# Performance work log

Hardware: AMD Instinct MI355X
Metric: run time of the kernel (lower is better)

The kernel has to match this reference:

```python
import jax, jax.numpy as jnp
import numpy as np

R_ITER = 3
EPS = 1e-7  # keras.backend.epsilon()


def squash(v, axis=-1):
    s2 = jnp.sum(jnp.square(v), axis=axis, keepdims=True)
    scale = s2 / (1.0 + s2) / jnp.sqrt(s2 + EPS)
    return scale * v


def setup_inputs() -> dict:
    key = jax.random.key(0)
    kx, kw = jax.random.split(key)
    B, N_IN, D_IN = 64, 2048, 8
    N_OUT, D_OUT = 32, 16
    x = jax.random.normal(kx, (B, N_IN, D_IN), dtype=jnp.float32)
    # W matches keras weight (1, N_IN//shared, N_OUT, D_OUT, D_IN) with shared=1,
    # stored here without the leading broadcast dim. RandomNormal(stddev=0.1).
    W = 0.1 * jax.random.normal(kw, (N_IN, N_OUT, D_OUT, D_IN), dtype=jnp.float32)
    return {"x": x, "W": W}


def reference(x, W):
    # predictions u_hat[b, i, j, :] = W[i, j] @ x[b, i]  -> [B, N_in, N_out, D_out]
    preds = jnp.einsum('nodi,bni->bnod', W, x)
    N_in, N_out = preds.shape[1], preds.shape[2]
    # raw routing logits start at zeros with broadcast batch dim (as in TF code)
    raw = jnp.zeros((1, N_in, N_out), dtype=x.dtype)
    for i in range(R_ITER):
        rw = jax.nn.softmax(raw, axis=2)                      # softmax over output caps
        s = jnp.sum(rw[..., None] * preds, axis=1)            # [B, N_out, D_out]
        v = squash(s, axis=-1)                                # squash over capsule dim
        if i < R_ITER - 1:
            # agreement: <u_hat_ij, v_j>
            raw = raw + jnp.einsum('bnod,bod->bno', preds, v)
    return v, rw
```

## Files before the change

kernel.cpp:

```cpp
#include <hip/hip_runtime.h>

static constexpr int B_    = 64;
static constexpr int N_    = 2048;
static constexpr int DI_   = 8;
static constexpr int O_    = 32;
static constexpr int P_    = 16;
static constexpr int OP_   = O_ * P_;
static constexpr int M_    = OP_ * B_;
static constexpr int CHUNK_ = 8;
static constexpr int NBLK_  = N_ / CHUNK_;

template <int MODE, bool ATOMIC>
__global__ __launch_bounds__(1024, 4)
void fused_pass(const float* __restrict__ x, const float* __restrict__ W,
                const float* __restrict__ v_in, float* __restrict__ s_out,
                float* __restrict__ rw_out) {
  __shared__ float x_lds[CHUNK_ * 8 * 65];
  __shared__ float a_lds[2][O_ * B_];
  const int tid  = threadIdx.x;
  const int lane = tid & 63;
  const int wave = tid >> 6;
  const int n0   = blockIdx.x * CHUNK_;

  #pragma unroll
  for (int k = 0; k < 4; ++k) {
    int d = k * 1024 + tid;
    int b = d >> 6, rem = d & 63;
    x_lds[rem * 65 + b] = x[b * (N_ * DI_) + n0 * DI_ + rem];
  }

  float s_r[32];
  #pragma unroll
  for (int q = 0; q < 32; ++q) s_r[q] = 0.0f;

  __syncthreads();

  #pragma unroll 1
  for (int nn = 0; nn < CHUNK_; ++nn) {
    const int n = n0 + nn;
    float xr[8];
    #pragma unroll
    for (int i = 0; i < 8; ++i) xr[i] = x_lds[(nn * 8 + i) * 65 + lane];

    float pr[2][16];
    float ao0 = 0.0f, ao1 = 0.0f;

    #pragma unroll
    for (int oo = 0; oo < 2; ++oo) {
      const int o_u = __builtin_amdgcn_readfirstlane(wave * 2 + oo);
      const float* wp = W + (size_t)(n * O_ + o_u) * (P_ * DI_);

      float4 va0, va1, va2, va3;
      if (MODE != 0) {
        const float4* vp =
            (const float4*)(v_in + (size_t)lane * OP_ + (wave * 2 + oo) * P_);
        va0 = vp[0]; va1 = vp[1]; va2 = vp[2]; va3 = vp[3];
      }

      float acc = 0.0f;
      #pragma unroll
      for (int p = 0; p < P_; ++p) {
        float pv = wp[p * 8 + 0] * xr[0];
        pv = __builtin_fmaf(wp[p * 8 + 1], xr[1], pv);
        pv = __builtin_fmaf(wp[p * 8 + 2], xr[2], pv);
        pv = __builtin_fmaf(wp[p * 8 + 3], xr[3], pv);
        pv = __builtin_fmaf(wp[p * 8 + 4], xr[4], pv);
        pv = __builtin_fmaf(wp[p * 8 + 5], xr[5], pv);
        pv = __builtin_fmaf(wp[p * 8 + 6], xr[6], pv);
        pv = __builtin_fmaf(wp[p * 8 + 7], xr[7], pv);
        if (MODE == 0) {
          s_r[oo * 16 + p] += pv;
        } else {
          pr[oo][p] = pv;
          const float vc = (p < 4)  ? ((p & 3) == 0 ? va0.x : (p & 3) == 1 ? va0.y : (p & 3) == 2 ? va0.z : va0.w)
                         : (p < 8)  ? ((p & 3) == 0 ? va1.x : (p & 3) == 1 ? va1.y : (p & 3) == 2 ? va1.z : va1.w)
                         : (p < 12) ? ((p & 3) == 0 ? va2.x : (p & 3) == 1 ? va2.y : (p & 3) == 2 ? va2.z : va2.w)
                                    : ((p & 3) == 0 ? va3.x : (p & 3) == 1 ? va3.y : (p & 3) == 2 ? va3.z : va3.w);
          acc = __builtin_fmaf(pv, vc, acc);
        }
      }
      if (MODE != 0) {
        if (oo == 0) ao0 = acc; else ao1 = acc;
        a_lds[nn & 1][(wave * 2 + oo) * B_ + lane] = acc;
      }
    }

    if (MODE != 0) {
      __syncthreads();

      float Z = 0.0f;
      #pragma unroll
      for (int o = 0; o < O_; ++o) Z += __expf(a_lds[nn & 1][o * B_ + lane]);
      const float rZ  = 1.0f / Z;
      const float rw0 = __expf(ao0) * rZ;
      const float rw1 = __expf(ao1) * rZ;

      #pragma unroll
      for (int p = 0; p < P_; ++p) {
        s_r[p]      = __builtin_fmaf(rw0, pr[0][p], s_r[p]);
        s_r[16 + p] = __builtin_fmaf(rw1, pr[1][p], s_r[16 + p]);
      }
      if (MODE == 2) {
        float2 t; t.x = rw0; t.y = rw1;
        *(float2*)(rw_out + ((size_t)lane * N_ + n) * O_ + wave * 2) = t;
      }
    }
  }

  if (ATOMIC) {
    #pragma unroll
    for (int oo = 0; oo < 2; ++oo) {
      float* sp = s_out + (size_t)((wave * 2 + oo) * P_) * B_ + lane;
      #pragma unroll
      for (int p = 0; p < P_; ++p) atomicAdd(&sp[p * B_], s_r[oo * 16 + p]);
    }
  } else {
    #pragma unroll
    for (int oo = 0; oo < 2; ++oo) {
      float* sp = s_out + (size_t)blockIdx.x * M_ +
                  (size_t)((wave * 2 + oo) * P_) * B_ + lane;
      #pragma unroll
      for (int p = 0; p < P_; ++p) sp[p * B_] = s_r[oo * 16 + p];
    }
  }
}

__global__ __launch_bounds__(1024)
void reduce1(const float* __restrict__ spart, float* __restrict__ p2, int K) {
  const int g  = blockIdx.x >> 4;
  const int mc = blockIdx.x & 15;
  const int kpg = K >> 4;
  const int m0 = mc * 2048 + threadIdx.x;
  float a0 = 0.0f, a1 = 0.0f;
  const float* p = spart + (size_t)(g * kpg) * M_;
  for (int k = 0; k < kpg; ++k) {
    a0 += p[(size_t)k * M_ + m0];
    a1 += p[(size_t)k * M_ + m0 + 1024];
  }
  p2[(size_t)g * M_ + m0]        = a0;
  p2[(size_t)g * M_ + m0 + 1024] = a1;
}

__global__ __launch_bounds__(1024)
void v_kernel(const float* __restrict__ src, int ngroups, float scale,
              const float* __restrict__ v_add, float* __restrict__ v_out,
              float* __restrict__ zero_buf) {
  __shared__ float sq[P_ * 64];
  const int t = threadIdx.x;
  const int b = t & 63;
  const int p = t >> 6;
  const int o = blockIdx.x;
  const int q = o * P_ + p;
  float acc = 0.0f;
  for (int g = 0; g < ngroups; ++g) acc += src[(size_t)g * M_ + q * 64 + b];
  acc *= scale;
  sq[p * 64 + b] = acc * acc;
  if (zero_buf) zero_buf[blockIdx.x * 1024 + t] = 0.0f;
  __syncthreads();
  float s2 = 0.0f;
  #pragma unroll
  for (int pp = 0; pp < P_; ++pp) s2 += sq[pp * 64 + b];
  float sc = (s2 / (1.0f + s2)) / sqrtf(s2 + 1e-7f);
  float v = acc * sc;
  const int idx = b * OP_ + q;
  v_out[idx] = v + (v_add ? v_add[idx] : 0.0f);
}

extern "C" void kernel_launch(void* const* d_in, const int* in_sizes, int n_in,
                              void* d_out, int out_size, void* d_ws, size_t ws_size,
                              hipStream_t stream) {
  (void)in_sizes; (void)n_in; (void)out_size;
  const float* x = (const float*)d_in[0];
  const float* W = (const float*)d_in[1];
  float* out_v  = (float*)d_out;
  float* out_rw = out_v + (size_t)B_ * O_ * P_;
  float* vws   = (float*)d_ws;
  float* vsum  = vws + M_;
  float* p2    = vsum + M_;
  float* spart = p2 + 16 * M_;

  const size_t need = (size_t)(2 * M_ + 16 * M_ + (size_t)NBLK_ * M_) * 4;

  dim3 gF(NBLK_), bF(1024), gV(O_), bV(1024), gR(256);
  if (ws_size >= need) {
    fused_pass<0, false><<<gF, bF, 0, stream>>>(x, W, nullptr, spart, nullptr);
    reduce1<<<gR, bF, 0, stream>>>(spart, p2, NBLK_);
    v_kernel<<<gV, bV, 0, stream>>>(p2, 16, 1.0f / 32.0f, nullptr, vws, nullptr);
    fused_pass<1, false><<<gF, bF, 0, stream>>>(x, W, vws, spart, nullptr);
    reduce1<<<gR, bF, 0, stream>>>(spart, p2, NBLK_);
    v_kernel<<<gV, bV, 0, stream>>>(p2, 16, 1.0f, vws, vsum, nullptr);
    fused_pass<2, false><<<gF, bF, 0, stream>>>(x, W, vsum, spart, out_rw);
    reduce1<<<gR, bF, 0, stream>>>(spart, p2, NBLK_);
    v_kernel<<<gV, bV, 0, stream>>>(p2, 16, 1.0f, nullptr, out_v, nullptr);
  } else {
    float* sAb = p2;
    float* sBb = sAb + M_;
    hipMemsetAsync(sAb, 0, (size_t)M_ * sizeof(float), stream);
    fused_pass<0, true><<<gF, bF, 0, stream>>>(x, W, nullptr, sAb, nullptr);
    v_kernel<<<gV, bV, 0, stream>>>(sAb, 1, 1.0f / 32.0f, nullptr, vws, sBb);
    fused_pass<1, true><<<gF, bF, 0, stream>>>(x, W, vws, sBb, nullptr);
    v_kernel<<<gV, bV, 0, stream>>>(sBb, 1, 1.0f, vws, vsum, sAb);
    fused_pass<2, true><<<gF, bF, 0, stream>>>(x, W, vsum, sAb, out_rw);
    v_kernel<<<gV, bV, 0, stream>>>(sAb, 1, 1.0f, nullptr, out_v, nullptr);
  }
}
```

Before: 272.5 us.

## Halve node chunk per block and restructure routing softmax to reuse exponentials

The softmax over output capsules now computes each exponential once per (n,o). The exp-weighted predictions are scaled by a single reciprocal of Z, where before each lane recomputed all 32 exponentials from the shared logits. In the first routing pass, waves store per-wave partial sums of exponentials, which shortens the Z reduction. The final pass writes each row of routing weights as contiguous float4 stores from one wave. The node chunk per block drops from 8 to 4, which doubles the block count but also doubles the partial-sum buffer that the reduction kernel must write and read.

```diff
diff --git a/kernel.cpp b/kernel.cpp
--- a/kernel.cpp
+++ b/kernel.cpp
@@ -7,7 +7,7 @@
 static constexpr int P_    = 16;
 static constexpr int OP_   = O_ * P_;
 static constexpr int M_    = OP_ * B_;
-static constexpr int CHUNK_ = 8;
+static constexpr int CHUNK_ = 4;
 static constexpr int NBLK_  = N_ / CHUNK_;
 
 template <int MODE, bool ATOMIC>
@@ -23,9 +23,9 @@
   const int n0   = blockIdx.x * CHUNK_;
 
   #pragma unroll
-  for (int k = 0; k < 4; ++k) {
+  for (int k = 0; k < 2; ++k) {
     int d = k * 1024 + tid;
-    int b = d >> 6, rem = d & 63;
+    int b = d >> 5, rem = d & 31;
     x_lds[rem * 65 + b] = x[b * (N_ * DI_) + n0 * DI_ + rem];
   }
 
@@ -42,8 +42,8 @@
     #pragma unroll
     for (int i = 0; i < 8; ++i) xr[i] = x_lds[(nn * 8 + i) * 65 + lane];
 
-    float pr[2][16];
-    float ao0 = 0.0f, ao1 = 0.0f;
+    float u[2][16];
+    float e0 = 0.0f, e1 = 0.0f;
 
     #pragma unroll
     for (int oo = 0; oo < 2; ++oo) {
@@ -71,7 +71,7 @@
         if (MODE == 0) {
           s_r[oo * 16 + p] += pv;
         } else {
-          pr[oo][p] = pv;
+          u[oo][p] = pv;
           const float vc = (p < 4)  ? ((p & 3) == 0 ? va0.x : (p & 3) == 1 ? va0.y : (p & 3) == 2 ? va0.z : va0.w)
                          : (p < 8)  ? ((p & 3) == 0 ? va1.x : (p & 3) == 1 ? va1.y : (p & 3) == 2 ? va1.z : va1.w)
                          : (p < 12) ? ((p & 3) == 0 ? va2.x : (p & 3) == 1 ? va2.y : (p & 3) == 2 ? va2.z : va2.w)
@@ -80,29 +80,50 @@
         }
       }
       if (MODE != 0) {
-        if (oo == 0) ao0 = acc; else ao1 = acc;
-        a_lds[nn & 1][(wave * 2 + oo) * B_ + lane] = acc;
+        const float e = __expf(acc);
+        if (oo == 0) e0 = e; else e1 = e;
+        #pragma unroll
+        for (int p = 0; p < P_; ++p) u[oo][p] *= e;
       }
     }
 
     if (MODE != 0) {
+      const int buf = nn & 1;
+      if (MODE == 1) {
+        a_lds[buf][wave * B_ + lane] = e0 + e1;
+      } else {
+        a_lds[buf][(wave * 2 + 0) * B_ + lane] = e0;
+        a_lds[buf][(wave * 2 + 1) * B_ + lane] = e1;
+      }
       __syncthreads();
 
       float Z = 0.0f;
-      #pragma unroll
-      for (int o = 0; o < O_; ++o) Z += __expf(a_lds[nn & 1][o * B_ + lane]);
-      const float rZ  = 1.0f / Z;
-      const float rw0 = __expf(ao0) * rZ;
-      const float rw1 = __expf(ao1) * rZ;
+      if (MODE == 1) {
+        #pragma unroll
+        for (int w = 0; w < 16; ++w) Z += a_lds[buf][w * B_ + lane];
+      } else {
+        #pragma unroll
+        for (int o = 0; o < O_; ++o) Z += a_lds[buf][o * B_ + lane];
+      }
+      const float rZ = __builtin_amdgcn_rcpf(Z);
 
       #pragma unroll
       for (int p = 0; p < P_; ++p) {
-        s_r[p]      = __builtin_fmaf(rw0, pr[0][p], s_r[p]);
-        s_r[16 + p] = __builtin_fmaf(rw1, pr[1][p], s_r[16 + p]);
-      }
-      if (MODE == 2) {
-        float2 t; t.x = rw0; t.y = rw1;
-        *(float2*)(rw_out + ((size_t)lane * N_ + n) * O_ + wave * 2) = t;
+        s_r[p]      = __builtin_fmaf(rZ, u[0][p], s_r[p]);
+        s_r[16 + p] = __builtin_fmaf(rZ, u[1][p], s_r[16 + p]);
+      }
+
+      if (MODE == 2 && wave == nn) {
+        float* rp = rw_out + ((size_t)lane * N_ + n) * O_;
+        #pragma unroll
+        for (int o4 = 0; o4 < 8; ++o4) {
+          float4 t;
+          t.x = a_lds[buf][(o4 * 4 + 0) * B_ + lane] * rZ;
+          t.y = a_lds[buf][(o4 * 4 + 1) * B_ + lane] * rZ;
+          t.z = a_lds[buf][(o4 * 4 + 2) * B_ + lane] * rZ;
+          t.w = a_lds[buf][(o4 * 4 + 3) * B_ + lane] * rZ;
+          ((float4*)rp)[o4] = t;
+        }
       }
     }
   }
```

Measured after the change: 312.7 us. +14.8%, slower.
